# Kernel tuning notes

Hardware: AMD Instinct MI355X
Metric: run time of the kernel (lower is better)

Reference implementation:

```python
import jax, jax.numpy as jnp
import numpy as np

B, S, D, H = 2, 2048, 1024, 16
HD = D // H  # head_dim = 64
ROPE_BASE = 10000.0


def _rope_cos_sin(seq_len, head_dim, dtype):
    inv_freq = 1.0 / (ROPE_BASE ** (jnp.arange(0, head_dim, 2, dtype=jnp.float32) / head_dim))
    t = jnp.arange(seq_len, dtype=jnp.float32)
    freqs = jnp.einsum('i,j->ij', t, inv_freq)            # [S, HD/2]
    emb = jnp.concatenate([freqs, freqs], axis=-1)        # [S, HD]
    return jnp.cos(emb).astype(dtype), jnp.sin(emb).astype(dtype)


def _rotate_half(x):
    x1, x2 = jnp.split(x, 2, axis=-1)
    return jnp.concatenate([-x2, x1], axis=-1)


def setup_inputs() -> dict:
    key = jax.random.key(0)
    ks = jax.random.split(key, 5)
    scale = 1.0 / np.sqrt(D)
    x = jax.random.normal(ks[0], (B, S, D), dtype=jnp.float32)
    wq = jax.random.normal(ks[1], (D, D), dtype=jnp.float32) * scale
    wk = jax.random.normal(ks[2], (D, D), dtype=jnp.float32) * scale
    wv = jax.random.normal(ks[3], (D, D), dtype=jnp.float32) * scale
    wo = jax.random.normal(ks[4], (D, D), dtype=jnp.float32) * scale
    # causal additive mask: 0 on/below diagonal, -1e9 above
    causal = jnp.triu(jnp.full((S, S), -1e9, dtype=jnp.float32), k=1)
    attention_mask = causal[None, None, :, :]
    return {'x': x, 'attention_mask': attention_mask, 'wq': wq, 'wk': wk, 'wv': wv, 'wo': wo}


def reference(x, attention_mask, wq, wk, wv, wo):
    b, s, d = x.shape
    scale = 1.0 / np.sqrt(HD)
    # projections (torch Linear: y = x @ W.T)
    q = (x @ wq.T).reshape(b, s, H, HD).transpose(0, 2, 1, 3)  # [B,H,S,HD]
    k = (x @ wk.T).reshape(b, s, H, HD).transpose(0, 2, 1, 3)
    v = (x @ wv.T).reshape(b, s, H, HD).transpose(0, 2, 1, 3)
    cos, sin = _rope_cos_sin(s, HD, x.dtype)                   # [S, HD]
    cos = cos[None, None]
    sin = sin[None, None]
    q = q * cos + _rotate_half(q) * sin
    k = k * cos + _rotate_half(k) * sin
    scores = jnp.einsum('bhqd,bhkd->bhqk', q, k) * scale       # [B,H,S,S]
    scores = scores + attention_mask
    probs = jax.nn.softmax(scores, axis=-1)
    out = jnp.einsum('bhqk,bhkd->bhqd', probs, v)              # [B,H,S,HD]
    out = out.transpose(0, 2, 1, 3).reshape(b, s, d)
    return out @ wo.T
```

## Files before the change

kernel.cpp:

```cpp
#include <hip/hip_runtime.h>
#include <cstdint>
#include <cstddef>

typedef __attribute__((ext_vector_type(8))) _Float16 half8;
typedef __attribute__((ext_vector_type(4))) _Float16 half4;
typedef __attribute__((ext_vector_type(4))) float f32x4;

#define NB 2
#define NS 2048
#define ND 1024
#define NH 16
#define NHD 64
#define NM (NB * NS)

__device__ __forceinline__ void cvt8(const float* __restrict__ s,
                                     _Float16* __restrict__ d, int g) {
  const float4* s4 = (const float4*)s + (size_t)g * 2;
  float4 a = s4[0], b = s4[1];
  half8 h;
  h[0] = (_Float16)a.x; h[1] = (_Float16)a.y;
  h[2] = (_Float16)a.z; h[3] = (_Float16)a.w;
  h[4] = (_Float16)b.x; h[5] = (_Float16)b.y;
  h[6] = (_Float16)b.z; h[7] = (_Float16)b.w;
  *(half8*)(d + (size_t)g * 8) = h;
}

__global__ void prep(const float* __restrict__ x,
                     const float* __restrict__ wq, const float* __restrict__ wk,
                     const float* __restrict__ wv, const float* __restrict__ wo,
                     _Float16* __restrict__ xb,
                     _Float16* __restrict__ wqb, _Float16* __restrict__ wkb,
                     _Float16* __restrict__ wvb, _Float16* __restrict__ wob,
                     float* __restrict__ cosT, float* __restrict__ sinT) {
  int i = blockIdx.x * 256 + threadIdx.x;
  if (i < 524288) {
    cvt8(x, xb, i);
  } else if (i < 1048576) {
    int j = i - 524288;
    int k = j >> 17, g = j & 131071;
    const float* ws = (k == 0) ? wq : (k == 1) ? wk : (k == 2) ? wv : wo;
    _Float16* wd = (k == 0) ? wqb : (k == 1) ? wkb : (k == 2) ? wvb : wob;
    cvt8(ws, wd, g);
  } else if (i < 1056768) {
    int t0 = (i - 1048576) * 8;
#pragma unroll
    for (int e = 0; e < 8; ++e) {
      int t = t0 + e;
      int s = t >> 5, j = t & 31;
      float inv = expf(-(float)(2 * j) * (9.210340371976184f / 64.0f));
      float ang = (float)s * inv;
      cosT[t] = cosf(ang);
      sinT[t] = sinf(ang);
    }
  }
}

__device__ __forceinline__ void gload_lds16(const void* g, void* lds) {
  __builtin_amdgcn_global_load_lds(
      (const __attribute__((address_space(1))) unsigned int*)g,
      (__attribute__((address_space(3))) unsigned int*)lds, 16, 0, 0);
}

__device__ __forceinline__ float exp2_fast(float x) {
  float r;
  asm("v_exp_f32 %0, %1" : "=v"(r) : "v"(x));
  return r;
}

__device__ __forceinline__ void gemm_mainloop(const _Float16* __restrict__ A,
                                              const _Float16* __restrict__ Bw,
                                              _Float16* As, _Float16* Bs,
                                              int brow, int bcol,
                                              int lane, int wid,
                                              f32x4 acc[4][4]) {
  const int l15 = lane & 15, l4 = lane >> 4;
  const int wr = wid >> 1, wc = wid & 1;
  const int srow = lane >> 2, scol = (lane & 3) * 8;
  const _Float16* Ab = A + (size_t)(brow + srow) * ND + scol;
  const _Float16* Bb = Bw + (size_t)(bcol + srow) * ND + scol;

  for (int kt = 0; kt < ND / 32; ++kt) {
    const int k0 = kt * 32;
#pragma unroll
    for (int c = 0; c < 2; ++c) {
      const int chunk = wid * 2 + c;
      gload_lds16(Ab + (size_t)chunk * 16 * ND + k0, As + chunk * 512);
      gload_lds16(Bb + (size_t)chunk * 16 * ND + k0, Bs + chunk * 512);
    }
    __syncthreads();
    half8 af[4], bf[4];
#pragma unroll
    for (int m = 0; m < 4; ++m)
      af[m] = *(const half8*)(As + (wr * 64 + m * 16 + l15) * 32 + l4 * 8);
#pragma unroll
    for (int n = 0; n < 4; ++n)
      bf[n] = *(const half8*)(Bs + (wc * 64 + n * 16 + l15) * 32 + l4 * 8);
#pragma unroll
    for (int m = 0; m < 4; ++m)
#pragma unroll
      for (int n = 0; n < 4; ++n)
        acc[m][n] = __builtin_amdgcn_mfma_f32_16x16x32_f16(af[m], bf[n],
                                                           acc[m][n], 0, 0, 0);
    __syncthreads();
  }
}

__launch_bounds__(256, 2)
__global__ void qkv_gemm(const _Float16* __restrict__ X,
                         const _Float16* __restrict__ Wq,
                         const _Float16* __restrict__ Wk,
                         const _Float16* __restrict__ Wv,
                         _Float16* __restrict__ Qb,
                         _Float16* __restrict__ Kb,
                         _Float16* __restrict__ Vt,
                         const float* __restrict__ cosT,
                         const float* __restrict__ sinT) {
  __shared__ __align__(16) _Float16 As[128 * 32];
  __shared__ __align__(16) _Float16 Bs[128 * 32];
  const int tid = threadIdx.x, lane = tid & 63, wid = tid >> 6;
  const int l15 = lane & 15, l4 = lane >> 4;
  const int wr = wid >> 1, wc = wid & 1;
  const int brow = blockIdx.y * 128, bcol = blockIdx.x * 128;
  const int mode = blockIdx.z;
  const _Float16* W = (mode == 0) ? Wq : (mode == 1 ? Wk : Wv);

  f32x4 acc[4][4] = {};
  gemm_mainloop(X, W, As, Bs, brow, bcol, lane, wid, acc);

  const int b = brow >> 11;
  const int sbase = (brow & (NS - 1)) + wr * 64;
  const int h = (bcol >> 6) + wc;

  if (mode < 2) {
    _Float16* oh = ((mode == 0) ? Qb : Kb) + (size_t)(b * NH + h) * NS * NHD;
#pragma unroll
    for (int m = 0; m < 4; ++m) {
#pragma unroll
      for (int r = 0; r < 4; ++r) {
        const int s = sbase + m * 16 + l4 * 4 + r;
#pragma unroll
        for (int n = 0; n < 2; ++n) {
          const int hd = n * 16 + l15;
          const float c = cosT[s * 32 + hd];
          const float sn = sinT[s * 32 + hd];
          const float lo = acc[m][n][r], hi = acc[m][n + 2][r];
          oh[(size_t)s * NHD + hd]      = (_Float16)(lo * c - hi * sn);
          oh[(size_t)s * NHD + hd + 32] = (_Float16)(hi * c + lo * sn);
        }
      }
    }
  } else {
#pragma unroll
    for (int m = 0; m < 4; ++m) {
      const int s0 = sbase + m * 16 + l4 * 4;
#pragma unroll
      for (int n = 0; n < 4; ++n) {
        const int hd = n * 16 + l15;
        half4 pk;
        pk[0] = (_Float16)acc[m][n][0];
        pk[1] = (_Float16)acc[m][n][1];
        pk[2] = (_Float16)acc[m][n][2];
        pk[3] = (_Float16)acc[m][n][3];
        *(half4*)(Vt + ((size_t)(b * NH + h) * NHD + hd) * NS + s0) = pk;
      }
    }
  }
}

__launch_bounds__(256, 2)
__global__ void flash_attn(const _Float16* __restrict__ Qb,
                           const _Float16* __restrict__ Kb,
                           const _Float16* __restrict__ Vt,
                           _Float16* __restrict__ Ob) {
  __shared__ __align__(16) _Float16 Ks[4][64 * 64];
  __shared__ __align__(16) _Float16 Vs[4][64 * 64];
  const int tid = threadIdx.x, lane = tid & 63, wid = tid >> 6;
  const int l15 = lane & 15, l4 = lane >> 4;
  const int bh = blockIdx.x & 31, pr = blockIdx.x >> 5;
  const _Float16* Qh = Qb + (size_t)bh * NS * NHD;
  const char* Kg = (const char*)(Kb + (size_t)bh * NS * NHD);
  const char* Vg = (const char*)(Vt + (size_t)bh * NHD * NS);

  const float K1 = 0.125f * 1.4426950408889634f;
  const int swz_lane = ((lane >> 3) & 7) << 4;
  const int qloc = wid * 16 + l15;
  const int rswz = (l15 & 7) << 4;
  const int b = bh >> 4, h = bh & 15;

  auto stage = [&](int kt, int si) {
#pragma unroll
    for (int c = 0; c < 2; ++c) {
      const int chunk = wid * 2 + c;
      const int slot = chunk * 1024 + lane * 16;
      const int sw = slot ^ swz_lane;
      gload_lds16(Kg + (size_t)kt * 8192 + sw, (char*)&Ks[si][0] + slot);
      const int vrow = slot >> 7;
      gload_lds16(Vg + (size_t)vrow * (NS * 2) + kt * 128 + (sw & 127),
                  (char*)&Vs[si][0] + slot);
    }
  };

  for (int item = 0; item < 2; ++item) {
    const int qt = item ? pr : 31 - pr;
    const int nkt = qt + 1;

    half8 qf[2];
#pragma unroll
    for (int kk = 0; kk < 2; ++kk)
      qf[kk] = *(const half8*)&Qh[(size_t)(qt * 64 + wid * 16 + l15) * NHD + kk * 32 + l4 * 8];

    f32x4 oacc[4] = {};
    float mrun = -3.0e38f, lrun = 0.f;

    stage(0, 0);
    if (nkt > 1) {
      stage(1, 1);
      asm volatile("s_waitcnt vmcnt(4)" ::: "memory");
    } else {
      asm volatile("s_waitcnt vmcnt(0)" ::: "memory");
    }
    __builtin_amdgcn_s_barrier();
    __builtin_amdgcn_sched_barrier(0);

    for (int kt = 0; kt < nkt; ++kt) {
      if (kt + 2 < nkt) stage(kt + 2, (kt + 2) & 3);

      const bool diag = (kt == qt);
      const char* Kbuf = (const char*)&Ks[kt & 3][0];
      const char* Vbuf = (const char*)&Vs[kt & 3][0];

      f32x4 sacc[4] = {};
      __builtin_amdgcn_s_setprio(1);
#pragma unroll
      for (int kk = 0; kk < 2; ++kk) {
#pragma unroll
        for (int n = 0; n < 4; ++n) {
          if (diag && n > wid) continue;
          const int off = ((n * 16 + l15) * 128 + kk * 64 + l4 * 16) ^ rswz;
          half8 kf = *(const half8*)(Kbuf + off);
          sacc[n] = __builtin_amdgcn_mfma_f32_16x16x32_f16(kf, qf[kk], sacc[n], 0, 0, 0);
        }
      }
      __builtin_amdgcn_s_setprio(0);

      float t[16];
#pragma unroll
      for (int n = 0; n < 4; ++n)
#pragma unroll
        for (int r = 0; r < 4; ++r) {
          float v = sacc[n][r] * K1;
          if (diag) {
            const int ki = n * 16 + l4 * 4 + r;
            v = (ki > qloc) ? -3.0e38f : v;
          }
          t[n * 4 + r] = v;
        }
      float mx = t[0];
#pragma unroll
      for (int j = 1; j < 16; ++j) mx = fmaxf(mx, t[j]);
      mx = fmaxf(mx, __shfl_xor(mx, 16, 64));
      mx = fmaxf(mx, __shfl_xor(mx, 32, 64));
      const float mnew = fmaxf(mrun, mx);
      const float alpha = exp2_fast(mrun - mnew);
      mrun = mnew;
      float ps[16], rs = 0.f;
#pragma unroll
      for (int j = 0; j < 16; ++j) {
        ps[j] = exp2_fast(t[j] - mnew);
        rs += ps[j];
      }
      rs += __shfl_xor(rs, 16, 64);
      rs += __shfl_xor(rs, 32, 64);
      lrun = lrun * alpha + rs;
#pragma unroll
      for (int n = 0; n < 4; ++n) {
        oacc[n][0] *= alpha; oacc[n][1] *= alpha;
        oacc[n][2] *= alpha; oacc[n][3] *= alpha;
      }

      __builtin_amdgcn_s_setprio(1);
#pragma unroll
      for (int c = 0; c < 2; ++c) {
        if (diag && c == 1 && wid < 2) continue;
        half8 pb;
#pragma unroll
        for (int j = 0; j < 8; ++j)
          pb[j] = (_Float16)ps[(2 * c + (j >> 2)) * 4 + (j & 3)];
#pragma unroll
        for (int n = 0; n < 4; ++n) {
          const int off0 = ((n * 16 + l15) * 128 + c * 64 + l4 * 8) ^ rswz;
          const int off1 = off0 ^ 32;
          half4 vlo = *(const half4*)(Vbuf + off0);
          half4 vhi = *(const half4*)(Vbuf + off1);
          half8 va;
          va[0] = vlo[0]; va[1] = vlo[1]; va[2] = vlo[2]; va[3] = vlo[3];
          va[4] = vhi[0]; va[5] = vhi[1]; va[6] = vhi[2]; va[7] = vhi[3];
          oacc[n] = __builtin_amdgcn_mfma_f32_16x16x32_f16(va, pb, oacc[n], 0, 0, 0);
        }
      }
      __builtin_amdgcn_s_setprio(0);

      if (kt + 2 < nkt) asm volatile("s_waitcnt vmcnt(4)" ::: "memory");
      else              asm volatile("s_waitcnt vmcnt(0)" ::: "memory");
      __builtin_amdgcn_s_barrier();
      __builtin_amdgcn_sched_barrier(0);
    }

    const int s = qt * 64 + wid * 16 + l15;
    const float invl = 1.0f / lrun;
#pragma unroll
    for (int n = 0; n < 4; ++n) {
      half4 o;
      o[0] = (_Float16)(oacc[n][0] * invl);
      o[1] = (_Float16)(oacc[n][1] * invl);
      o[2] = (_Float16)(oacc[n][2] * invl);
      o[3] = (_Float16)(oacc[n][3] * invl);
      *(half4*)&Ob[((size_t)(b * NS + s)) * ND + h * NHD + n * 16 + l4 * 4] = o;
    }
  }
}

__launch_bounds__(256, 2)
__global__ void proj_gemm(const _Float16* __restrict__ A,
                          const _Float16* __restrict__ W,
                          float* __restrict__ out) {
  __shared__ __align__(16) _Float16 As[128 * 32];
  __shared__ __align__(16) _Float16 Bs[128 * 32];
  const int tid = threadIdx.x, lane = tid & 63, wid = tid >> 6;
  const int l15 = lane & 15, l4 = lane >> 4;
  const int wr = wid >> 1, wc = wid & 1;
  const int brow = blockIdx.y * 128, bcol = blockIdx.x * 128;
  f32x4 acc[4][4] = {};
  gemm_mainloop(A, W, As, Bs, brow, bcol, lane, wid, acc);
#pragma unroll
  for (int m = 0; m < 4; ++m)
#pragma unroll
    for (int n = 0; n < 4; ++n)
#pragma unroll
      for (int r = 0; r < 4; ++r)
        out[(size_t)(brow + wr * 64 + m * 16 + l4 * 4 + r) * ND
            + bcol + wc * 64 + n * 16 + l15] = acc[m][n][r];
}

extern "C" void kernel_launch(void* const* d_in, const int* in_sizes, int n_in,
                              void* d_out, int out_size, void* d_ws, size_t ws_size,
                              hipStream_t stream) {
  const float* x  = (const float*)d_in[0];
  const float* wq = (const float*)d_in[2];
  const float* wk = (const float*)d_in[3];
  const float* wv = (const float*)d_in[4];
  const float* wo = (const float*)d_in[5];
  float* out = (float*)d_out;

  char* w = (char*)d_ws;
  _Float16* xb   = (_Float16*)(w);
  _Float16* wqb  = (_Float16*)(w + (8ull  << 20));
  _Float16* wkb  = (_Float16*)(w + (10ull << 20));
  _Float16* wvb  = (_Float16*)(w + (12ull << 20));
  _Float16* wob  = (_Float16*)(w + (14ull << 20));
  _Float16* Qb   = (_Float16*)(w + (16ull << 20));
  _Float16* Kb   = (_Float16*)(w + (24ull << 20));
  _Float16* Vt   = (_Float16*)(w + (32ull << 20));
  _Float16* Ob   = (_Float16*)(w + (40ull << 20));
  float*    cosT = (float*)   (w + (48ull << 20));
  float*    sinT = (float*)   (w + (48ull << 20) + (1ull << 18));

  dim3 blk(256);
  prep<<<4128, blk, 0, stream>>>(x, wq, wk, wv, wo, xb, wqb, wkb, wvb, wob,
                                 cosT, sinT);
  qkv_gemm<<<dim3(8, 32, 3), blk, 0, stream>>>(xb, wqb, wkb, wvb, Qb, Kb, Vt,
                                               cosT, sinT);
  flash_attn<<<512, blk, 0, stream>>>(Qb, Kb, Vt, Ob);
  proj_gemm<<<dim3(8, 32), blk, 0, stream>>>(Ob, wob, out);
}
```

Before: 110.8 us.

## Software-pipeline QK^T of next tile with softmax and PV of current tile

```diff
diff --git a/kernel.cpp b/kernel.cpp
--- a/kernel.cpp
+++ b/kernel.cpp
@@ -213,42 +213,64 @@
     float mrun = -3.0e38f, lrun = 0.f;
 
     stage(0, 0);
-    if (nkt > 1) {
-      stage(1, 1);
-      asm volatile("s_waitcnt vmcnt(4)" ::: "memory");
-    } else {
-      asm volatile("s_waitcnt vmcnt(0)" ::: "memory");
-    }
+    if (nkt > 1) stage(1, 1);
+    asm volatile("s_waitcnt vmcnt(0)" ::: "memory");
     __builtin_amdgcn_s_barrier();
     __builtin_amdgcn_sched_barrier(0);
 
-    for (int kt = 0; kt < nkt; ++kt) {
-      if (kt + 2 < nkt) stage(kt + 2, (kt + 2) & 3);
-
-      const bool diag = (kt == qt);
-      const char* Kbuf = (const char*)&Ks[kt & 3][0];
-      const char* Vbuf = (const char*)&Vs[kt & 3][0];
-
-      f32x4 sacc[4] = {};
+    f32x4 scur[4] = {};
+    {
+      const char* Kbuf = (const char*)&Ks[0][0];
+      const bool d0 = (qt == 0);
       __builtin_amdgcn_s_setprio(1);
 #pragma unroll
       for (int kk = 0; kk < 2; ++kk) {
 #pragma unroll
         for (int n = 0; n < 4; ++n) {
-          if (diag && n > wid) continue;
+          if (d0 && n > wid) continue;
           const int off = ((n * 16 + l15) * 128 + kk * 64 + l4 * 16) ^ rswz;
           half8 kf = *(const half8*)(Kbuf + off);
-          sacc[n] = __builtin_amdgcn_mfma_f32_16x16x32_f16(kf, qf[kk], sacc[n], 0, 0, 0);
+          scur[n] = __builtin_amdgcn_mfma_f32_16x16x32_f16(kf, qf[kk], scur[n], 0, 0, 0);
         }
       }
       __builtin_amdgcn_s_setprio(0);
+    }
+
+    for (int kt = 0; kt < nkt; ++kt) {
+      const bool diag = (kt == qt);
+      const bool havenext = (kt + 1 < nkt);
+      if (kt + 2 < nkt) stage(kt + 2, (kt + 2) & 3);
+
+      half8 kfn[2][4];
+      if (havenext) {
+        const char* Kb2 = (const char*)&Ks[(kt + 1) & 3][0];
+#pragma unroll
+        for (int kk = 0; kk < 2; ++kk)
+#pragma unroll
+          for (int n = 0; n < 4; ++n) {
+            const int off = ((n * 16 + l15) * 128 + kk * 64 + l4 * 16) ^ rswz;
+            kfn[kk][n] = *(const half8*)(Kb2 + off);
+          }
+      }
+      half4 vlo[2][4], vhi[2][4];
+      {
+        const char* Vbuf = (const char*)&Vs[kt & 3][0];
+#pragma unroll
+        for (int c = 0; c < 2; ++c)
+#pragma unroll
+          for (int n = 0; n < 4; ++n) {
+            const int off0 = ((n * 16 + l15) * 128 + c * 64 + l4 * 8) ^ rswz;
+            vlo[c][n] = *(const half4*)(Vbuf + off0);
+            vhi[c][n] = *(const half4*)(Vbuf + (off0 ^ 32));
+          }
+      }
 
       float t[16];
 #pragma unroll
       for (int n = 0; n < 4; ++n)
 #pragma unroll
         for (int r = 0; r < 4; ++r) {
-          float v = sacc[n][r] * K1;
+          float v = scur[n][r] * K1;
           if (diag) {
             const int ki = n * 16 + l4 * 4 + r;
             v = (ki > qloc) ? -3.0e38f : v;
@@ -278,6 +300,20 @@
         oacc[n][2] *= alpha; oacc[n][3] *= alpha;
       }
 
+      f32x4 snext[4] = {};
+      if (havenext) {
+        const bool dn = (kt + 1 == qt);
+        __builtin_amdgcn_s_setprio(1);
+#pragma unroll
+        for (int kk = 0; kk < 2; ++kk)
+#pragma unroll
+          for (int n = 0; n < 4; ++n) {
+            if (dn && n > wid) continue;
+            snext[n] = __builtin_amdgcn_mfma_f32_16x16x32_f16(kfn[kk][n], qf[kk], snext[n], 0, 0, 0);
+          }
+        __builtin_amdgcn_s_setprio(0);
+      }
+
       __builtin_amdgcn_s_setprio(1);
 #pragma unroll
       for (int c = 0; c < 2; ++c) {
@@ -288,22 +324,22 @@
           pb[j] = (_Float16)ps[(2 * c + (j >> 2)) * 4 + (j & 3)];
 #pragma unroll
         for (int n = 0; n < 4; ++n) {
-          const int off0 = ((n * 16 + l15) * 128 + c * 64 + l4 * 8) ^ rswz;
-          const int off1 = off0 ^ 32;
-          half4 vlo = *(const half4*)(Vbuf + off0);
-          half4 vhi = *(const half4*)(Vbuf + off1);
           half8 va;
-          va[0] = vlo[0]; va[1] = vlo[1]; va[2] = vlo[2]; va[3] = vlo[3];
-          va[4] = vhi[0]; va[5] = vhi[1]; va[6] = vhi[2]; va[7] = vhi[3];
+          va[0] = vlo[c][n][0]; va[1] = vlo[c][n][1];
+          va[2] = vlo[c][n][2]; va[3] = vlo[c][n][3];
+          va[4] = vhi[c][n][0]; va[5] = vhi[c][n][1];
+          va[6] = vhi[c][n][2]; va[7] = vhi[c][n][3];
           oacc[n] = __builtin_amdgcn_mfma_f32_16x16x32_f16(va, pb, oacc[n], 0, 0, 0);
         }
       }
       __builtin_amdgcn_s_setprio(0);
 
-      if (kt + 2 < nkt) asm volatile("s_waitcnt vmcnt(4)" ::: "memory");
-      else              asm volatile("s_waitcnt vmcnt(0)" ::: "memory");
+      asm volatile("s_waitcnt vmcnt(0)" ::: "memory");
       __builtin_amdgcn_s_barrier();
       __builtin_amdgcn_sched_barrier(0);
+
+#pragma unroll
+      for (int n = 0; n < 4; ++n) scur[n] = snext[n];
     }
 
     const int s = qt * 64 + wid * 16 + l15;
```

Result: no change. 112.6 us (+1.6%).
